# Optimization experiments

Hardware: AMD Instinct MI355X
Metric: run time of the kernel (lower is better)

## Reference

```python
import jax, jax.numpy as jnp
import numpy as np

FRAME_PERIOD = 80
SAMPLE_RATE = 16000
FFT_LENGTH = 1024
DEFAULT_F0 = 500.0
Q1 = -0.15
F_MIN = 3.0 * SAMPLE_RATE / (FFT_LENGTH - 3)
TAU = 2.0 * np.pi
SAFEGUARD = 1e-12  # noise floor added to windowed waveform
L1 = FFT_LENGTH // 2 + 1  # one-sided spectrum length
RATE = SAMPLE_RATE / FFT_LENGTH  # Hz per FFT bin
PAD = 64  # mirror padding (bins) for linear smoothing; > max half-width 500Hz/(3*RATE)~10.7


def setup_inputs() -> dict:
    key = jax.random.key(0)
    k1, k2 = jax.random.split(key)
    B, T = 8, 160000
    N = T // FRAME_PERIOD + 1  # 2001 frames
    x = jax.random.normal(k1, (B, T), jnp.float32)
    # realistic speech pitch range 100..300 Hz (all > F_MIN=47 Hz)
    f0 = 100.0 + 200.0 * jax.random.uniform(k2, (B, N), jnp.float32)
    return {"x": x, "f0": f0}


def _windowed_waveform(x, f0):
    # x: (B,T), f0: (B,N,1). Pitch-adaptive Hanning window (3 periods), WORLD-style.
    B, T = x.shape
    N = f0.shape[1]
    base = jnp.arange(FFT_LENGTH) - FFT_LENGTH // 2  # (L,)
    half_len = jnp.round(1.5 * SAMPLE_RATE / f0)  # (B,N,1) half window length in samples
    mask = (jnp.abs(base) <= half_len).astype(x.dtype)  # (B,N,L)
    window = (0.5 * jnp.cos(np.pi * (base / (1.5 * SAMPLE_RATE)) * f0) + 0.5) * mask
    centers = jnp.arange(N) * FRAME_PERIOD  # frame centers in samples
    idx = jnp.clip(centers[:, None] + base[None, :], 0, T - 1)  # (N,L)
    seg = x[:, idx]  # (B,N,L)
    noise = jax.random.normal(jax.random.key(1234), (B, N, FFT_LENGTH), x.dtype)
    w = seg * window + noise * SAFEGUARD * mask
    # remove window-weighted mean (zero DC)
    w = w - window * (jnp.sum(w, -1, keepdims=True) / jnp.sum(window, -1, keepdims=True))
    return w


def _dc_correction(ps, f0):
    # add mirrored low-frequency replica below f0 (WORLD DCCorrection)
    k = jnp.arange(L1)
    pos = f0 / RATE - k  # fractional bin of mirror frequency f0 - f, (B,N,L1)
    lo = jnp.clip(jnp.floor(pos).astype(jnp.int32), 0, L1 - 2)
    fr = pos - lo
    rep = (jnp.take_along_axis(ps, lo, -1) * (1.0 - fr)
           + jnp.take_along_axis(ps, lo + 1, -1) * fr)
    return ps + jnp.where(k * RATE < f0, rep, 0.0)


def _linear_smoothing(ps, width):
    # rectangular smoothing of width `width` Hz via cumulative integral (WORLD LinearSmoothing)
    e = jnp.arange(-PAD, L1 + PAD)
    j = jnp.abs(e)
    j = jnp.where(j > L1 - 1, 2 * (L1 - 1) - j, j)  # mirror-reflected bin indices
    ext = ps[..., j]  # (B,N,L1+2*PAD)
    C = jnp.cumsum(ext, -1) * RATE
    C = jnp.concatenate([jnp.zeros(C.shape[:-1] + (1,), C.dtype), C], -1)

    def interp(q):
        lo = jnp.clip(jnp.floor(q).astype(jnp.int32), 0, C.shape[-1] - 2)
        fr = q - lo
        return (jnp.take_along_axis(C, lo, -1) * (1.0 - fr)
                + jnp.take_along_axis(C, lo + 1, -1) * fr)

    k = jnp.arange(L1).astype(ps.dtype)
    hwb = width / (2.0 * RATE)  # half-width in bins, (B,N,1)
    q_hi = k + hwb + PAD + 0.5
    q_lo = k - hwb + PAD + 0.5
    return (interp(q_hi) - interp(q_lo)) / width


def _forward(x, f0):
    f0 = jnp.where(f0 <= F_MIN, DEFAULT_F0, f0)[..., None]  # (B,N,1)
    f0 = jax.lax.stop_gradient(f0)  # original code calls .detach()
    w = _windowed_waveform(x, f0)
    ps = jnp.abs(jnp.fft.rfft(w, n=FFT_LENGTH)) ** 2  # (B,N,L1)
    ps = _dc_correction(ps, f0)
    ps = _linear_smoothing(ps, f0 * (2.0 / 3.0))
    ps = ps + jnp.abs(jax.random.normal(jax.random.key(4321), ps.shape, ps.dtype)) * jnp.finfo(x.dtype).eps
    quefrency = jnp.arange(L1) / SAMPLE_RATE
    z = f0 * quefrency  # (B,N,L1)
    smoothing_lifter = jnp.sinc(z).at[..., 0].set(1.0)
    compensation_lifter = 1.0 - 2.0 * Q1 + 2.0 * Q1 * jnp.cos(TAU * z)
    cepstrum = jnp.fft.irfft(jnp.log(ps).astype(jnp.complex64), n=FFT_LENGTH)[..., :L1]
    lifted = (cepstrum * smoothing_lifter * compensation_lifter).astype(jnp.complex64)
    log_power_spectrum = jnp.fft.hfft(lifted, n=FFT_LENGTH)[..., :L1]
    return log_power_spectrum.astype(x.dtype)


def reference(x, f0):
    return _forward(x, f0)
```

## Files before the change

### kernel.cpp

```cpp
#include <hip/hip_runtime.h>
#include <math.h>

#define PI_F 3.14159265358979323846f

__device__ __forceinline__ void fft512(float* Ar, float* Ai, float* Br, float* Bi,
                                       const float2* TW, int t) {
  float* xr = Ar; float* xi = Ai; float* yr = Br; float* yi = Bi;
#pragma unroll
  for (int s = 0; s < 9; ++s) {
    __syncthreads();
    const int m = 1 << s;
    float ar = xr[t],       ai = xi[t];
    float br = xr[t + 256], bi = xi[t + 256];
    float2 w = TW[t & ~(m - 1)];
    int o = t + (t & ~(m - 1));
    float sr = ar - br, si = ai - bi;
    yr[o] = ar + br;            yi[o] = ai + bi;
    yr[o + m] = sr * w.x + si * w.y;
    yi[o + m] = si * w.x - sr * w.y;
    float* tp;
    tp = xr; xr = yr; yr = tp;
    tp = xi; xi = yi; yi = tp;
  }
  __syncthreads();
}

__device__ __forceinline__ float unpack_re(const float* Br, const float* Bi,
                                           const float2* UP, int k) {
  int kk = k & 511, kr = (512 - k) & 511;
  float zr = Br[kk], zi = Bi[kk];
  float ur = Br[kr], ui = Bi[kr];
  float Er = 0.5f * (zr + ur);
  float Or = 0.5f * (zi + ui), Oi = 0.5f * (ur - zr);
  float2 w = UP[k];
  return Er + w.x * Or + w.y * Oi;
}

__device__ __forceinline__ float unpack_pwr(const float* Br, const float* Bi,
                                            const float2* UP, int k) {
  int kk = k & 511, kr = (512 - k) & 511;
  float zr = Br[kk], zi = Bi[kk];
  float ur = Br[kr], ui = Bi[kr];
  float Er = 0.5f * (zr + ur), Ei = 0.5f * (zi - ui);
  float Or = 0.5f * (zi + ui), Oi = 0.5f * (ur - zr);
  float2 w = UP[k];
  float re = Er + w.x * Or + w.y * Oi;
  float im = Ei + w.x * Oi - w.y * Or;
  return re * re + im * im;
}

__global__ __launch_bounds__(256)
void cheaptrick_kernel(const float* __restrict__ x, const float* __restrict__ f0g,
                       float* __restrict__ out, int Tlen, int Nfr) {
  __shared__ float Ar[512], Ai[512], Br[512], Bi[512];
  __shared__ float ps[513];
  __shared__ float C[642];
  __shared__ float red[16];
  __shared__ float2 TW[256];
  __shared__ float2 UP[513];

  const int t = threadIdx.x;
  const int blk = blockIdx.x;
  const int b = blk / Nfr;
  const int n = blk - b * Nfr;
  const int lane = t & 63, wave = t >> 6;
  const float RATE = 15.625f;

  {
    float sn, cs;
    sincosf((PI_F / 256.0f) * (float)t, &sn, &cs);
    TW[t] = make_float2(cs, sn);
    sincosf((PI_F / 512.0f) * (float)t, &sn, &cs);
    UP[t] = make_float2(cs, sn);
    sincosf((PI_F / 512.0f) * (float)(t + 257), &sn, &cs);
    UP[t + 257] = make_float2(cs, sn);
    if (t == 0) UP[256] = make_float2(0.0f, 1.0f);
  }

  float f0v = f0g[blk];
  const float F_MIN = 3.0f * 16000.0f / 1021.0f;
  if (f0v <= F_MIN) f0v = 500.0f;

  float half_len = rintf(24000.0f / f0v);
  float wv[4], wd[4];
  float sw = 0.f, swin = 0.f;
  const int center = n * 80;
  const int ids[4] = {2 * t, 2 * t + 1, 2 * t + 512, 2 * t + 513};
#pragma unroll
  for (int q = 0; q < 4; ++q) {
    int base = ids[q] - 512;
    float fb = (float)base;
    float msk = (fabsf(fb) <= half_len) ? 1.0f : 0.0f;
    float win = (0.5f * __cosf(PI_F * (fb / 24000.0f) * f0v) + 0.5f) * msk;
    int src = center + base;
    src = min(max(src, 0), Tlen - 1);
    float wval = x[(size_t)b * (size_t)Tlen + src] * win;
    wd[q] = win; wv[q] = wval;
    sw += wval; swin += win;
  }
#pragma unroll
  for (int off = 32; off > 0; off >>= 1) {
    sw += __shfl_down(sw, off);
    swin += __shfl_down(swin, off);
  }
  if (lane == 0) { red[wave] = sw; red[4 + wave] = swin; }
  __syncthreads();
  float mf = (red[0] + red[1] + red[2] + red[3]) / (red[4] + red[5] + red[6] + red[7]);

  Ar[t]       = wv[0] - wd[0] * mf;
  Ai[t]       = wv[1] - wd[1] * mf;
  Ar[t + 256] = wv[2] - wd[2] * mf;
  Ai[t + 256] = wv[3] - wd[3] * mf;

  fft512(Ar, Ai, Br, Bi, TW, t);

  {
    float p0 = unpack_pwr(Br, Bi, UP, t);
    float p1 = unpack_pwr(Br, Bi, UP, t + 256);
    float p2 = (t == 0) ? unpack_pwr(Br, Bi, UP, 512) : 0.f;
    ps[t] = p0; ps[t + 256] = p1;
    if (t == 0) ps[512] = p2;
  }
  __syncthreads();

  {
    float rep = 0.f;
    bool act = (t < 40);
    float kf = (float)t;
    if (act) {
      float pos = f0v / RATE - kf;
      int lo = (int)floorf(pos);
      lo = min(max(lo, 0), 511);
      float fr = pos - (float)lo;
      rep = ps[lo] * (1.0f - fr) + ps[lo + 1] * fr;
    }
    __syncthreads();
    if (act && kf * RATE < f0v) ps[t] += rep;
  }
  __syncthreads();

  {
    const int ebase = 3 * t;
    float e0 = 0.f, e1 = 0.f, e2 = 0.f;
    {
      int e = ebase;
      if (e < 641)     { int j = e - 64;     j = j < 0 ? -j : j; if (j > 512) j = 1024 - j; e0 = ps[j]; }
      if (e + 1 < 641) { int j = e + 1 - 64; j = j < 0 ? -j : j; if (j > 512) j = 1024 - j; e1 = ps[j]; }
      if (e + 2 < 641) { int j = e + 2 - 64; j = j < 0 ? -j : j; if (j > 512) j = 1024 - j; e2 = ps[j]; }
    }
    float psum = e0 + e1 + e2;
    float sc = psum;
#pragma unroll
    for (int off = 1; off < 64; off <<= 1) {
      float v = __shfl_up(sc, off);
      if (lane >= off) sc += v;
    }
    if (lane == 63) red[8 + wave] = sc;
    __syncthreads();
    float woff = 0.f;
#pragma unroll
    for (int w2 = 0; w2 < 4; ++w2) woff += (w2 < wave) ? red[8 + w2] : 0.f;
    float run = woff + (sc - psum);
    if (t == 0) C[0] = 0.f;
    if (ebase < 641)     { run += e0; C[ebase + 1] = RATE * run; }
    if (ebase + 1 < 641) { run += e1; C[ebase + 2] = RATE * run; }
    if (ebase + 2 < 641) { run += e2; C[ebase + 3] = RATE * run; }
  }
  __syncthreads();

  {
    const float width = f0v * (2.0f / 3.0f);
    const float hwb = width * (1.0f / (2.0f * RATE));
    const float winv = 1.0f / width;
    float s0, s1, s2 = 1.f;
#pragma unroll
    for (int r = 0; r < 3; ++r) {
      int k = (r == 0) ? t : (r == 1) ? (t + 256) : 512;
      if (r == 2 && t != 0) break;
      float kf = (float)k;
      float qh = kf + hwb + 64.5f, ql = kf - hwb + 64.5f;
      int lh = (int)floorf(qh); lh = min(max(lh, 0), 640);
      int ll = (int)floorf(ql); ll = min(max(ll, 0), 640);
      float fh = qh - (float)lh, fl = ql - (float)ll;
      float vh = C[lh] * (1.f - fh) + C[lh + 1] * fh;
      float vl = C[ll] * (1.f - fl) + C[ll + 1] * fl;
      float v = (vh - vl) * winv;
      if (r == 0) s0 = v; else if (r == 1) s1 = v; else s2 = v;
    }
    ps[t] = __logf(s0);
    ps[t + 256] = __logf(s1);
    if (t == 0) ps[512] = __logf(s2);
  }
  __syncthreads();

  Ar[t]       = ps[2 * t];
  Ai[t]       = ps[2 * t + 1];
  Ar[t + 256] = ps[(2 * t + 512) <= 512 ? (2 * t + 512) : (1024 - (2 * t + 512))];
  Ai[t + 256] = ps[1024 - (2 * t + 513)];
  fft512(Ar, Ai, Br, Bi, TW, t);

  {
    const float inv = 1.0f / 1024.0f;
    float l0, l1, l2 = 0.f;
#pragma unroll
    for (int r = 0; r < 3; ++r) {
      int k = (r == 0) ? t : (r == 1) ? (t + 256) : 512;
      if (r == 2 && t != 0) break;
      float cep = unpack_re(Br, Bi, UP, k) * inv;
      float z = f0v * ((float)k * (1.0f / 16000.0f));
      float pz = PI_F * z;
      float s = __sinf(pz);
      float sl = (k == 0) ? 1.0f : (s / pz);
      float cl = 1.0f + 0.6f * s * s;
      float v = cep * sl * cl;
      if (r == 0) l0 = v; else if (r == 1) l1 = v; else l2 = v;
    }
    ps[t] = l0; ps[t + 256] = l1;
    if (t == 0) ps[512] = l2;
  }
  __syncthreads();

  Ar[t]       = ps[2 * t];
  Ai[t]       = ps[2 * t + 1];
  Ar[t + 256] = ps[(2 * t + 512) <= 512 ? (2 * t + 512) : (1024 - (2 * t + 512))];
  Ai[t + 256] = ps[1024 - (2 * t + 513)];
  fft512(Ar, Ai, Br, Bi, TW, t);

  {
    size_t ob = (size_t)blk * 513;
    out[ob + t]       = unpack_re(Br, Bi, UP, t);
    out[ob + t + 256] = unpack_re(Br, Bi, UP, t + 256);
    if (t == 0) out[ob + 512] = unpack_re(Br, Bi, UP, 512);
  }
}

extern "C" void kernel_launch(void* const* d_in, const int* in_sizes, int n_in,
                              void* d_out, int out_size, void* d_ws, size_t ws_size,
                              hipStream_t stream) {
  (void)n_in; (void)d_ws; (void)ws_size; (void)out_size;
  const float* x  = (const float*)d_in[0];
  const float* f0 = (const float*)d_in[1];
  float* out = (float*)d_out;
  int B = in_sizes[1] - in_sizes[0] / 80;
  if (B < 1) B = 1;
  int Tlen = in_sizes[0] / B;
  int Nfr  = in_sizes[1] / B;
  dim3 grid(in_sizes[1]), block(256);
  hipLaunchKernelGGL(cheaptrick_kernel, grid, block, 0, stream, x, f0, out, Tlen, Nfr);
}
```

Baseline: 176.2 us.

## Register-resident FFT with wave shuffles, padded LDS and precomputed twiddle tables

Replaces the 9-stage shared-memory ping-pong FFT with a register-resident radix-2 FFT. The first two stages go through padded LDS and the remaining stages use intra-wave __shfl_xor exchanges with twiddles derived by rotation, which cuts barriers and LDS traffic per FFT. Bin-reversed, bank-padded indexing (PSI/RVP) is used for the spectrum buffers, input samples are loaded as float4, and twiddle tables are computed once by a separate init kernel into workspace instead of per-block sincosf. In exchange it adds a second kernel launch, extra index arithmetic for bit reversal, and twiddles that carry small rotation rounding error.

```diff
diff --git a/kernel.cpp b/kernel.cpp
--- a/kernel.cpp
+++ b/kernel.cpp
@@ -3,61 +3,133 @@
 
 #define PI_F 3.14159265358979323846f
 
-__device__ __forceinline__ void fft512(float* Ar, float* Ai, float* Br, float* Bi,
-                                       const float2* TW, int t) {
-  float* xr = Ar; float* xi = Ai; float* yr = Br; float* yi = Bi;
-#pragma unroll
-  for (int s = 0; s < 9; ++s) {
-    __syncthreads();
-    const int m = 1 << s;
-    float ar = xr[t],       ai = xi[t];
-    float br = xr[t + 256], bi = xi[t + 256];
-    float2 w = TW[t & ~(m - 1)];
-    int o = t + (t & ~(m - 1));
-    float sr = ar - br, si = ai - bi;
-    yr[o] = ar + br;            yi[o] = ai + bi;
-    yr[o + m] = sr * w.x + si * w.y;
-    yi[o + m] = si * w.x - sr * w.y;
-    float* tp;
-    tp = xr; xr = yr; yr = tp;
-    tp = xi; xi = yi; yi = tp;
-  }
-  __syncthreads();
-}
-
-__device__ __forceinline__ float unpack_re(const float* Br, const float* Bi,
-                                           const float2* UP, int k) {
+__device__ __forceinline__ int PSI(int i) { return i + (i >> 5); }
+__device__ __forceinline__ int RVP(int v) {
+  int r = (int)(__brev((unsigned)v) >> 23);
+  return r + (r >> 5);
+}
+
+#define BFLY(cr, ci, pr, pi, vs, wx, wy) do {            \
+    float sr_ = (vs) ? ((pr) - (cr)) : ((pr) + (cr));    \
+    float si_ = (vs) ? ((pi) - (ci)) : ((pi) + (ci));    \
+    float ex_ = (vs) ? (wx) : 1.0f;                      \
+    float ey_ = (vs) ? (wy) : 0.0f;                      \
+    (cr) = sr_ * ex_ + si_ * ey_;                        \
+    (ci) = si_ * ex_ - sr_ * ey_;                        \
+  } while (0)
+
+#define SHUF_STAGE(d, h, CH, SH) do {                                   \
+    float p0r = __shfl_xor(c0r, h); float p0i = __shfl_xor(c0i, h);     \
+    float p1r = __shfl_xor(c1r, h); float p1i = __shfl_xor(c1i, h);     \
+    bool vs = (t & (h)) != 0;                                           \
+    int m0 = ((2 * t) & ((d) - 1)) * (256 / (d));                       \
+    float w0x = TWc[m0], w0y = TWs[m0];                                 \
+    float w1x = w0x * (CH) - w0y * (SH);                                \
+    float w1y = w0y * (CH) + w0x * (SH);                                \
+    BFLY(c0r, c0i, p0r, p0i, vs, w0x, w0y);                             \
+    BFLY(c1r, c1i, p1r, p1i, vs, w1x, w1y);                             \
+  } while (0)
+
+__device__ __forceinline__ void fft512r(float& c0r, float& c0i, float& c1r, float& c1i,
+                                        float* Zr, float* Zi,
+                                        const float* TWc, const float* TWs, int t) {
+  const int i0 = PSI(2 * t);
+  Zr[i0] = c0r; Zr[i0 + 1] = c1r;
+  Zi[i0] = c0i; Zi[i0 + 1] = c1i;
+  __syncthreads();
+  {
+    int pp = PSI((2 * t) ^ 256);
+    float p0r = Zr[pp], p0i = Zi[pp];
+    float p1r = Zr[pp + 1], p1i = Zi[pp + 1];
+    bool vs = (t & 128) != 0;
+    int m0 = (2 * t) & 255;
+    float w0x = TWc[m0], w0y = TWs[m0];
+    const float CH = 0.99992470183914450f, SH = 0.01227153828571993f;
+    float w1x = w0x * CH - w0y * SH, w1y = w0y * CH + w0x * SH;
+    BFLY(c0r, c0i, p0r, p0i, vs, w0x, w0y);
+    BFLY(c1r, c1i, p1r, p1i, vs, w1x, w1y);
+  }
+  __syncthreads();
+  Zr[i0] = c0r; Zr[i0 + 1] = c1r;
+  Zi[i0] = c0i; Zi[i0 + 1] = c1i;
+  __syncthreads();
+  {
+    int pp = PSI((2 * t) ^ 128);
+    float p0r = Zr[pp], p0i = Zi[pp];
+    float p1r = Zr[pp + 1], p1i = Zi[pp + 1];
+    bool vs = (t & 64) != 0;
+    int m0 = ((2 * t) & 127) * 2;
+    float w0x = TWc[m0], w0y = TWs[m0];
+    const float CH = 0.99969881869620420f, SH = 0.02454122852291229f;
+    float w1x = w0x * CH - w0y * SH, w1y = w0y * CH + w0x * SH;
+    BFLY(c0r, c0i, p0r, p0i, vs, w0x, w0y);
+    BFLY(c1r, c1i, p1r, p1i, vs, w1x, w1y);
+  }
+  SHUF_STAGE(64, 32, 0.99879545620517240f, 0.04906767432741802f);
+  SHUF_STAGE(32, 16, 0.99518472667219690f, 0.09801714032956060f);
+  SHUF_STAGE(16, 8,  0.98078528040323040f, 0.19509032201612825f);
+  SHUF_STAGE(8, 4,   0.92387953251128670f, 0.38268343236508980f);
+  SHUF_STAGE(4, 2,   0.70710678118654750f, 0.70710678118654750f);
+  SHUF_STAGE(2, 1,   0.0f, 1.0f);
+  {
+    float ar = c0r, ai = c0i;
+    c0r = ar + c1r; c0i = ai + c1i;
+    c1r = ar - c1r; c1i = ai - c1i;
+  }
+  __syncthreads();
+  Zr[i0] = c0r; Zr[i0 + 1] = c1r;
+  Zi[i0] = c0i; Zi[i0 + 1] = c1i;
+  __syncthreads();
+}
+
+__device__ __forceinline__ float unpack_pwr(const float* Zr, const float* Zi,
+                                            const float* UPc, const float* UPs, int k) {
   int kk = k & 511, kr = (512 - k) & 511;
-  float zr = Br[kk], zi = Bi[kk];
-  float ur = Br[kr], ui = Bi[kr];
+  int a = RVP(kk), c = RVP(kr);
+  float zr = Zr[a], zi = Zi[a];
+  float ur = Zr[c], ui = Zi[c];
+  float Er = 0.5f * (zr + ur), Ei = 0.5f * (zi - ui);
+  float Or = 0.5f * (zi + ui), Oi = 0.5f * (ur - zr);
+  float wx = UPc[k], wy = UPs[k];
+  float re = Er + wx * Or + wy * Oi;
+  float im = Ei + wx * Oi - wy * Or;
+  return re * re + im * im;
+}
+
+__device__ __forceinline__ float unpack_re(const float* Zr, const float* Zi,
+                                           const float* UPc, const float* UPs, int k) {
+  int kk = k & 511, kr = (512 - k) & 511;
+  int a = RVP(kk), c = RVP(kr);
+  float zr = Zr[a], zi = Zi[a];
+  float ur = Zr[c], ui = Zi[c];
   float Er = 0.5f * (zr + ur);
   float Or = 0.5f * (zi + ui), Oi = 0.5f * (ur - zr);
-  float2 w = UP[k];
-  return Er + w.x * Or + w.y * Oi;
-}
-
-__device__ __forceinline__ float unpack_pwr(const float* Br, const float* Bi,
-                                            const float2* UP, int k) {
-  int kk = k & 511, kr = (512 - k) & 511;
-  float zr = Br[kk], zi = Bi[kk];
-  float ur = Br[kr], ui = Bi[kr];
-  float Er = 0.5f * (zr + ur), Ei = 0.5f * (zi - ui);
-  float Or = 0.5f * (zi + ui), Oi = 0.5f * (ur - zr);
-  float2 w = UP[k];
-  float re = Er + w.x * Or + w.y * Oi;
-  float im = Ei + w.x * Oi - w.y * Or;
-  return re * re + im * im;
+  float wx = UPc[k], wy = UPs[k];
+  return Er + wx * Or + wy * Oi;
+}
+
+__global__ __launch_bounds__(256) void init_tables(float* __restrict__ w) {
+  int i = blockIdx.x * 256 + threadIdx.x;
+  if (i < 256) {
+    float sn, cs; sincosf((PI_F / 256.0f) * (float)i, &sn, &cs);
+    w[i] = cs; w[256 + i] = sn;
+  } else if (i < 769) {
+    int k = i - 256;
+    float sn, cs; sincosf((PI_F / 512.0f) * (float)k, &sn, &cs);
+    w[512 + k] = cs; w[1025 + k] = sn;
+  }
 }
 
 __global__ __launch_bounds__(256)
 void cheaptrick_kernel(const float* __restrict__ x, const float* __restrict__ f0g,
-                       float* __restrict__ out, int Tlen, int Nfr) {
-  __shared__ float Ar[512], Ai[512], Br[512], Bi[512];
-  __shared__ float ps[513];
+                       float* __restrict__ out, int Tlen, int Nfr,
+                       const float* __restrict__ tw) {
+  __shared__ float Zr[528], Zi[528];
+  __shared__ float ps[530];
   __shared__ float C[642];
   __shared__ float red[16];
-  __shared__ float2 TW[256];
-  __shared__ float2 UP[513];
+  __shared__ float TWc[256], TWs[256];
+  __shared__ float UPc[513], UPs[513];
 
   const int t = threadIdx.x;
   const int blk = blockIdx.x;
@@ -66,15 +138,17 @@
   const int lane = t & 63, wave = t >> 6;
   const float RATE = 15.625f;
 
-  {
+  if (tw) {
+    TWc[t] = tw[t];             TWs[t] = tw[256 + t];
+    UPc[t] = tw[512 + t];       UPs[t] = tw[1025 + t];
+    UPc[t + 257] = tw[769 + t]; UPs[t + 257] = tw[1282 + t];
+    if (t == 0) { UPc[256] = tw[768]; UPs[256] = tw[1281]; }
+  } else {
     float sn, cs;
-    sincosf((PI_F / 256.0f) * (float)t, &sn, &cs);
-    TW[t] = make_float2(cs, sn);
-    sincosf((PI_F / 512.0f) * (float)t, &sn, &cs);
-    UP[t] = make_float2(cs, sn);
-    sincosf((PI_F / 512.0f) * (float)(t + 257), &sn, &cs);
-    UP[t + 257] = make_float2(cs, sn);
-    if (t == 0) UP[256] = make_float2(0.0f, 1.0f);
+    sincosf((PI_F / 256.0f) * (float)t, &sn, &cs); TWc[t] = cs; TWs[t] = sn;
+    sincosf((PI_F / 512.0f) * (float)t, &sn, &cs); UPc[t] = cs; UPs[t] = sn;
+    sincosf((PI_F / 512.0f) * (float)(t + 257), &sn, &cs); UPc[t + 257] = cs; UPs[t + 257] = sn;
+    if (t == 0) { UPc[256] = 0.0f; UPs[256] = 1.0f; }
   }
 
   float f0v = f0g[blk];
@@ -82,19 +156,27 @@
   if (f0v <= F_MIN) f0v = 500.0f;
 
   float half_len = rintf(24000.0f / f0v);
+  const int center = n * 80;
+  const float* xb = x + (size_t)b * (size_t)Tlen;
+  const int s0 = center - 512 + 4 * t;
+  float xq[4];
+  if (s0 >= 0 && s0 + 3 < Tlen) {
+    const float4 f4 = *reinterpret_cast<const float4*>(xb + s0);
+    xq[0] = f4.x; xq[1] = f4.y; xq[2] = f4.z; xq[3] = f4.w;
+  } else {
+    xq[0] = xb[min(max(s0, 0), Tlen - 1)];
+    xq[1] = xb[min(max(s0 + 1, 0), Tlen - 1)];
+    xq[2] = xb[min(max(s0 + 2, 0), Tlen - 1)];
+    xq[3] = xb[min(max(s0 + 3, 0), Tlen - 1)];
+  }
   float wv[4], wd[4];
   float sw = 0.f, swin = 0.f;
-  const int center = n * 80;
-  const int ids[4] = {2 * t, 2 * t + 1, 2 * t + 512, 2 * t + 513};
 #pragma unroll
   for (int q = 0; q < 4; ++q) {
-    int base = ids[q] - 512;
-    float fb = (float)base;
+    float fb = (float)(4 * t + q - 512);
     float msk = (fabsf(fb) <= half_len) ? 1.0f : 0.0f;
     float win = (0.5f * __cosf(PI_F * (fb / 24000.0f) * f0v) + 0.5f) * msk;
-    int src = center + base;
-    src = min(max(src, 0), Tlen - 1);
-    float wval = x[(size_t)b * (size_t)Tlen + src] * win;
+    float wval = xq[q] * win;
     wd[q] = win; wv[q] = wval;
     sw += wval; swin += win;
   }
@@ -107,20 +189,14 @@
   __syncthreads();
   float mf = (red[0] + red[1] + red[2] + red[3]) / (red[4] + red[5] + red[6] + red[7]);
 
-  Ar[t]       = wv[0] - wd[0] * mf;
-  Ai[t]       = wv[1] - wd[1] * mf;
-  Ar[t + 256] = wv[2] - wd[2] * mf;
-  Ai[t + 256] = wv[3] - wd[3] * mf;
-
-  fft512(Ar, Ai, Br, Bi, TW, t);
-
-  {
-    float p0 = unpack_pwr(Br, Bi, UP, t);
-    float p1 = unpack_pwr(Br, Bi, UP, t + 256);
-    float p2 = (t == 0) ? unpack_pwr(Br, Bi, UP, 512) : 0.f;
-    ps[t] = p0; ps[t + 256] = p1;
-    if (t == 0) ps[512] = p2;
-  }
+  float c0r = wv[0] - wd[0] * mf, c0i = wv[1] - wd[1] * mf;
+  float c1r = wv[2] - wd[2] * mf, c1i = wv[3] - wd[3] * mf;
+
+  fft512r(c0r, c0i, c1r, c1i, Zr, Zi, TWc, TWs, t);
+
+  ps[PSI(t)] = unpack_pwr(Zr, Zi, UPc, UPs, t);
+  ps[PSI(t + 256)] = unpack_pwr(Zr, Zi, UPc, UPs, t + 256);
+  if (t == 0) ps[PSI(512)] = unpack_pwr(Zr, Zi, UPc, UPs, 512);
   __syncthreads();
 
   {
@@ -132,10 +208,10 @@
       int lo = (int)floorf(pos);
       lo = min(max(lo, 0), 511);
       float fr = pos - (float)lo;
-      rep = ps[lo] * (1.0f - fr) + ps[lo + 1] * fr;
+      rep = ps[PSI(lo)] * (1.0f - fr) + ps[PSI(lo + 1)] * fr;
     }
     __syncthreads();
-    if (act && kf * RATE < f0v) ps[t] += rep;
+    if (act && kf * RATE < f0v) ps[PSI(t)] += rep;
   }
   __syncthreads();
 
@@ -144,9 +220,9 @@
     float e0 = 0.f, e1 = 0.f, e2 = 0.f;
     {
       int e = ebase;
-      if (e < 641)     { int j = e - 64;     j = j < 0 ? -j : j; if (j > 512) j = 1024 - j; e0 = ps[j]; }
-      if (e + 1 < 641) { int j = e + 1 - 64; j = j < 0 ? -j : j; if (j > 512) j = 1024 - j; e1 = ps[j]; }
-      if (e + 2 < 641) { int j = e + 2 - 64; j = j < 0 ? -j : j; if (j > 512) j = 1024 - j; e2 = ps[j]; }
+      if (e < 641)     { int j = e - 64;     j = j < 0 ? -j : j; if (j > 512) j = 1024 - j; e0 = ps[PSI(j)]; }
+      if (e + 1 < 641) { int j = e + 1 - 64; j = j < 0 ? -j : j; if (j > 512) j = 1024 - j; e1 = ps[PSI(j)]; }
+      if (e + 2 < 641) { int j = e + 2 - 64; j = j < 0 ? -j : j; if (j > 512) j = 1024 - j; e2 = ps[PSI(j)]; }
     }
     float psum = e0 + e1 + e2;
     float sc = psum;
@@ -172,7 +248,7 @@
     const float width = f0v * (2.0f / 3.0f);
     const float hwb = width * (1.0f / (2.0f * RATE));
     const float winv = 1.0f / width;
-    float s0, s1, s2 = 1.f;
+    float s0v, s1v, s2v = 1.f;
 #pragma unroll
     for (int r = 0; r < 3; ++r) {
       int k = (r == 0) ? t : (r == 1) ? (t + 256) : 512;
@@ -185,19 +261,24 @@
       float vh = C[lh] * (1.f - fh) + C[lh + 1] * fh;
       float vl = C[ll] * (1.f - fl) + C[ll + 1] * fl;
       float v = (vh - vl) * winv;
-      if (r == 0) s0 = v; else if (r == 1) s1 = v; else s2 = v;
-    }
-    ps[t] = __logf(s0);
-    ps[t + 256] = __logf(s1);
-    if (t == 0) ps[512] = __logf(s2);
-  }
-  __syncthreads();
-
-  Ar[t]       = ps[2 * t];
-  Ai[t]       = ps[2 * t + 1];
-  Ar[t + 256] = ps[(2 * t + 512) <= 512 ? (2 * t + 512) : (1024 - (2 * t + 512))];
-  Ai[t + 256] = ps[1024 - (2 * t + 513)];
-  fft512(Ar, Ai, Br, Bi, TW, t);
+      if (r == 0) s0v = v; else if (r == 1) s1v = v; else s2v = v;
+    }
+    ps[PSI(t)] = __logf(s0v);
+    ps[PSI(t + 256)] = __logf(s1v);
+    if (t == 0) ps[PSI(512)] = __logf(s2v);
+  }
+  __syncthreads();
+
+  if (t < 128) {
+    int bse = 4 * t;
+    c0r = ps[PSI(bse)];     c0i = ps[PSI(bse + 1)];
+    c1r = ps[PSI(bse + 2)]; c1i = ps[PSI(bse + 3)];
+  } else {
+    int bse = 1024 - 4 * t;
+    c0r = ps[PSI(bse)];     c0i = ps[PSI(bse - 1)];
+    c1r = ps[PSI(bse - 2)]; c1i = ps[PSI(bse - 3)];
+  }
+  fft512r(c0r, c0i, c1r, c1i, Zr, Zi, TWc, TWs, t);
 
   {
     const float inv = 1.0f / 1024.0f;
@@ -206,7 +287,7 @@
     for (int r = 0; r < 3; ++r) {
       int k = (r == 0) ? t : (r == 1) ? (t + 256) : 512;
       if (r == 2 && t != 0) break;
-      float cep = unpack_re(Br, Bi, UP, k) * inv;
+      float cep = unpack_re(Zr, Zi, UPc, UPs, k) * inv;
       float z = f0v * ((float)k * (1.0f / 16000.0f));
       float pz = PI_F * z;
       float s = __sinf(pz);
@@ -215,29 +296,34 @@
       float v = cep * sl * cl;
       if (r == 0) l0 = v; else if (r == 1) l1 = v; else l2 = v;
     }
-    ps[t] = l0; ps[t + 256] = l1;
-    if (t == 0) ps[512] = l2;
-  }
-  __syncthreads();
-
-  Ar[t]       = ps[2 * t];
-  Ai[t]       = ps[2 * t + 1];
-  Ar[t + 256] = ps[(2 * t + 512) <= 512 ? (2 * t + 512) : (1024 - (2 * t + 512))];
-  Ai[t + 256] = ps[1024 - (2 * t + 513)];
-  fft512(Ar, Ai, Br, Bi, TW, t);
+    ps[PSI(t)] = l0; ps[PSI(t + 256)] = l1;
+    if (t == 0) ps[PSI(512)] = l2;
+  }
+  __syncthreads();
+
+  if (t < 128) {
+    int bse = 4 * t;
+    c0r = ps[PSI(bse)];     c0i = ps[PSI(bse + 1)];
+    c1r = ps[PSI(bse + 2)]; c1i = ps[PSI(bse + 3)];
+  } else {
+    int bse = 1024 - 4 * t;
+    c0r = ps[PSI(bse)];     c0i = ps[PSI(bse - 1)];
+    c1r = ps[PSI(bse - 2)]; c1i = ps[PSI(bse - 3)];
+  }
+  fft512r(c0r, c0i, c1r, c1i, Zr, Zi, TWc, TWs, t);
 
   {
     size_t ob = (size_t)blk * 513;
-    out[ob + t]       = unpack_re(Br, Bi, UP, t);
-    out[ob + t + 256] = unpack_re(Br, Bi, UP, t + 256);
-    if (t == 0) out[ob + 512] = unpack_re(Br, Bi, UP, 512);
+    out[ob + t]       = unpack_re(Zr, Zi, UPc, UPs, t);
+    out[ob + t + 256] = unpack_re(Zr, Zi, UPc, UPs, t + 256);
+    if (t == 0) out[ob + 512] = unpack_re(Zr, Zi, UPc, UPs, 512);
   }
 }
 
 extern "C" void kernel_launch(void* const* d_in, const int* in_sizes, int n_in,
                               void* d_out, int out_size, void* d_ws, size_t ws_size,
                               hipStream_t stream) {
-  (void)n_in; (void)d_ws; (void)ws_size; (void)out_size;
+  (void)n_in; (void)out_size;
   const float* x  = (const float*)d_in[0];
   const float* f0 = (const float*)d_in[1];
   float* out = (float*)d_out;
@@ -245,6 +331,12 @@
   if (B < 1) B = 1;
   int Tlen = in_sizes[0] / B;
   int Nfr  = in_sizes[1] / B;
-  dim3 grid(in_sizes[1]), block(256);
-  hipLaunchKernelGGL(cheaptrick_kernel, grid, block, 0, stream, x, f0, out, Tlen, Nfr);
-}
+
+  float* tw = nullptr;
+  if (d_ws && ws_size >= 1538 * sizeof(float)) {
+    tw = (float*)d_ws;
+    hipLaunchKernelGGL(init_tables, dim3(4), dim3(256), 0, stream, tw);
+  }
+  hipLaunchKernelGGL(cheaptrick_kernel, dim3(in_sizes[1]), dim3(256), 0, stream,
+                     x, f0, out, Tlen, Nfr, (const float*)tw);
+}
```

After: 220.1 us. 1.25x slower.
